# Performance work log

Hardware: AMD Instinct MI355X
Metric: run time of the kernel (lower is better)

The kernel has to match this reference:

```python
import jax, jax.numpy as jnp
import numpy as np

B, C, H, W = 32, 512, 32, 32
D = C // 8

def setup_inputs() -> dict:
    key = jax.random.key(0)
    ks = jax.random.split(key, 5)
    return {
        "x": jax.random.normal(ks[0], (B, C, H, W), dtype=jnp.float32),
        "w1": jax.random.normal(ks[1], (D, C), dtype=jnp.float32) * (1.0 / np.sqrt(C)),
        "b1": jax.random.normal(ks[2], (D,), dtype=jnp.float32) * 0.01,
        "w2": jax.random.normal(ks[3], (C, C), dtype=jnp.float32) * (1.0 / np.sqrt(C)),
        "b2": jax.random.normal(ks[4], (C,), dtype=jnp.float32) * 0.01,
    }

def reference(x, w1, b1, w2, b2):
    b, c, h, w = x.shape
    n = h * w
    xf = x.reshape(b, c, n)                                   # [B,C,N]
    # 1x1 convs == channel-mixing GEMMs; conv1 is shared for q and k
    qk = jnp.einsum('bcn,dc->bdn', xf, w1) + b1[None, :, None]  # [B,D,N]
    v = jnp.einsum('bcn,oc->bon', xf, w2) + b2[None, :, None]   # [B,C,N]
    q = qk.transpose(0, 2, 1)                                 # [B,N,D]
    attn = jax.nn.softmax(jnp.einsum('bnd,bdm->bnm', q, qk), axis=-1)  # [B,N,N]
    out = jnp.einsum('bnm,bcm->bnc', attn, v)                 # [B,N,C]
    # Faithful quirk: original views [B,N,C] directly as [B,C,H,W] (no transpose)
    return x + out.reshape(b, c, h, w)
```

## Files before the change

### kernel.cpp

```cpp
#include <hip/hip_runtime.h>
#include <hip/hip_bf16.h>
#include <math.h>

#define B_ 32
#define C_ 512
#define N_ 1024
#define D_ 64
#define OPAD 640

typedef __attribute__((ext_vector_type(4))) float f32x4;
typedef __attribute__((ext_vector_type(4))) float float4v;
typedef __attribute__((ext_vector_type(8))) __bf16 bf16x8;

#define MFMA16(a, b, c) __builtin_amdgcn_mfma_f32_16x16x32_bf16((a), (b), (c), 0, 0, 0)

__device__ inline void load_lds16(const void* g, void* l) {
    __builtin_amdgcn_global_load_lds(
        (const __attribute__((address_space(1))) void*)g,
        (__attribute__((address_space(3))) void*)l, 16, 0, 0);
}

__global__ void k_cast_weights(const float* __restrict__ w1,
                               const float* __restrict__ w2,
                               __hip_bfloat16* __restrict__ Wbf) {
    int idx = blockIdx.x * 256 + threadIdx.x;
    if (idx >= OPAD * C_) return;
    int m = idx >> 9;
    int k = idx & (C_ - 1);
    float val = (m < D_) ? w1[m * C_ + k]
              : (m < D_ + C_) ? w2[(m - D_) * C_ + k] : 0.0f;
    Wbf[idx] = __float2bfloat16(val);
}

__global__ __launch_bounds__(256) void k_transpose_cast(
        const float* __restrict__ x, __hip_bfloat16* __restrict__ xT) {
    __shared__ float tile[64][68];
    int b = blockIdx.z;
    int n0 = blockIdx.x * 64;
    int c0 = blockIdx.y * 64;
    int t = threadIdx.x;
    const float* xb = x + (size_t)b * (C_ * N_);
#pragma unroll
    for (int i = 0; i < 4; i++) {
        int c = i * 16 + (t >> 4);
        int nc = (t & 15) * 4;
        *(float4v*)&tile[c][nc] =
            *(const float4v*)(xb + (size_t)(c0 + c) * N_ + n0 + nc);
    }
    __syncthreads();
    __hip_bfloat16* xTb = xT + (size_t)b * (N_ * C_);
#pragma unroll
    for (int i = 0; i < 2; i++) {
        int n = i * 32 + (t >> 3);
        int cs = (t & 7) * 8;
        alignas(16) __hip_bfloat16 tmp[8];
#pragma unroll
        for (int j = 0; j < 8; j++)
            tmp[j] = __float2bfloat16(tile[cs + j][n]);
        *(bf16x8*)(xTb + (size_t)(n0 + n) * C_ + c0 + cs) = *(bf16x8*)tmp;
    }
}

__global__ __launch_bounds__(256) void k_gemm_qkv(
        const __hip_bfloat16* __restrict__ Wbf,
        const __hip_bfloat16* __restrict__ xT,
        const float* __restrict__ b1, const float* __restrict__ b2,
        __hip_bfloat16* __restrict__ qkT, __hip_bfloat16* __restrict__ v) {
    __shared__ __hip_bfloat16 As[128 * 64];
    __shared__ __hip_bfloat16 Bs[128 * 64];
    __shared__ __hip_bfloat16 epi[4][16][72];
    int b = blockIdx.x;
    int t = threadIdx.x;
    int wave = t >> 6, lane = t & 63, lr = lane & 15, quad = lane >> 4;
    int wm = wave >> 1, wn = wave & 1;
    int m_blk = blockIdx.z * 128;
    int n_blk = blockIdx.y * 128;
    const __hip_bfloat16* xTb = xT + (size_t)b * (N_ * C_);

    f32x4 acc[4][4] = {};
    for (int kk = 0; kk < C_; kk += 64) {
#pragma unroll
        for (int i = 0; i < 4; i++) {
            int id = i * 256 + t;
            int r = id >> 3, cx = id & 7;
            int gc = cx ^ (r & 7);
            load_lds16(Wbf + (size_t)(m_blk + r) * C_ + kk + gc * 8, &As[id * 8]);
            load_lds16(xTb + (size_t)(n_blk + r) * C_ + kk + gc * 8, &Bs[id * 8]);
        }
        __syncthreads();
#pragma unroll
        for (int h = 0; h < 2; h++) {
            bf16x8 af[4], bfr[4];
#pragma unroll
            for (int i = 0; i < 4; i++) {
                int ra = wm * 64 + i * 16 + lr;
                int rb = wn * 64 + i * 16 + lr;
                int q = h * 4 + quad;
                af[i]  = *(const bf16x8*)&As[ra * 64 + (q ^ (lr & 7)) * 8];
                bfr[i] = *(const bf16x8*)&Bs[rb * 64 + (q ^ (lr & 7)) * 8];
            }
#pragma unroll
            for (int mt = 0; mt < 4; mt++)
#pragma unroll
                for (int nt = 0; nt < 4; nt++)
                    acc[mt][nt] = MFMA16(af[mt], bfr[nt], acc[mt][nt]);
        }
        __syncthreads();
    }

#pragma unroll
    for (int mt = 0; mt < 4; mt++) {
        int m_frag = m_blk + wm * 64 + mt * 16;
        if (m_frag >= D_ + C_) continue;
        int m0 = m_frag + quad * 4;
        if (m_frag < D_) {
#pragma unroll
            for (int nt = 0; nt < 4; nt++) {
                int n = n_blk + wn * 64 + nt * 16 + lr;
                alignas(8) __hip_bfloat16 tmp[4];
#pragma unroll
                for (int r = 0; r < 4; r++)
                    tmp[r] = __float2bfloat16(acc[mt][nt][r] + b1[m0 + r]);
                *reinterpret_cast<short4*>(qkT + ((size_t)b * N_ + n) * D_ + m0) =
                    *reinterpret_cast<short4*>(tmp);
            }
        } else {
#pragma unroll
            for (int nt = 0; nt < 4; nt++) {
#pragma unroll
                for (int r = 0; r < 4; r++) {
                    int c = m0 - D_ + r;
                    epi[wave][quad * 4 + r][nt * 16 + lr] =
                        __float2bfloat16(acc[mt][nt][r] + b2[c]);
                }
            }
            int cbase = m_frag - D_;
            int row = lane >> 2;
#pragma unroll
            for (int it = 0; it < 2; it++) {
                int col = it * 32 + (lane & 3) * 8;
                bf16x8 frag = *(const bf16x8*)&epi[wave][row][col];
                *(bf16x8*)(v + (size_t)(b * C_ + cbase + row) * N_
                             + n_blk + wn * 64 + col) = frag;
            }
        }
    }
}

__global__ __launch_bounds__(512, 2) void k_fused_attn(
        const __hip_bfloat16* __restrict__ qkT,
        const __hip_bfloat16* __restrict__ v,
        const float* __restrict__ x, float* __restrict__ out) {
    __shared__ char smem[155648];
    __hip_bfloat16* Ks  = (__hip_bfloat16*)smem;
    __hip_bfloat16* Vs0 = (__hip_bfloat16*)(smem + 8192);
    __hip_bfloat16* Vs1 = (__hip_bfloat16*)(smem + 73728);
    __hip_bfloat16* Ps  = (__hip_bfloat16*)(smem + 139264);
    float* Obuf = (float*)smem;
    float* Rs   = (float*)(smem + 66560);

    int b = blockIdx.x;
    int t = threadIdx.x;
    int wave = t >> 6, lane = t & 63, lr = lane & 15, quad = lane >> 4;
    int wm = wave >> 2, wn = wave & 3;
    int n_blk = blockIdx.y * 128;
    const __hip_bfloat16* qb = qkT + (size_t)b * (N_ * D_);
    const __hip_bfloat16* vb = v + (size_t)b * (C_ * N_);

    {
        int r = t >> 3, cxx = t & 7, gc = cxx ^ (r & 7);
        load_lds16(qb + (size_t)r * D_ + gc * 8, &Ks[t * 8]);
    }
#pragma unroll
    for (int i = 0; i < 8; i++) {
        int id = i * 512 + t;
        int r = id >> 3, cxx = id & 7, gc = cxx ^ (r & 7);
        load_lds16(vb + (size_t)r * N_ + gc * 8, &Vs0[id * 8]);
    }

    union bfu { bf16x8 v; __hip_bfloat16 h[8]; };
    bf16x8 bq[2];
    float shift;
    {
        int nq = n_blk + wave * 16 + lr;
        bq[0] = *(const bf16x8*)(qb + (size_t)nq * D_ + quad * 8);
        bq[1] = *(const bf16x8*)(qb + (size_t)nq * D_ + 32 + quad * 8);
        float sq = 0.f;
#pragma unroll
        for (int dh = 0; dh < 2; dh++) {
            bfu u; u.v = bq[dh];
#pragma unroll
            for (int j = 0; j < 8; j++) {
                float qv = __bfloat162float(u.h[j]);
                sq += qv * qv;
            }
        }
        sq += __shfl_xor(sq, 16);
        sq += __shfl_xor(sq, 32);
        shift = sq;
    }

    f32x4 acc[4][8] = {};
    float rsum = 0.f;

    __syncthreads();

    for (int tt = 0; tt < 16; ++tt) {
        int kk = tt * 64;
        __hip_bfloat16* Vcur = (tt & 1) ? Vs1 : Vs0;
        __hip_bfloat16* Vnxt = (tt & 1) ? Vs0 : Vs1;

        if (tt < 15) {
#pragma unroll
            for (int i = 0; i < 8; i++) {
                int id = i * 512 + t;
                int r = id >> 3, cxx = id & 7, gc = cxx ^ (r & 7);
                load_lds16(vb + (size_t)r * N_ + kk + 64 + gc * 8, &Vnxt[id * 8]);
            }
        }

#pragma unroll
        for (int mi = 0; mi < 4; mi++) {
            int m = mi * 16 + lr;
            bf16x8 ak0 = *(const bf16x8*)&Ks[m * 64 + ((quad) ^ (lr & 7)) * 8];
            bf16x8 ak1 = *(const bf16x8*)&Ks[m * 64 + ((4 + quad) ^ (lr & 7)) * 8];
            f32x4 s = {};
            s = MFMA16(ak0, bq[0], s);
            s = MFMA16(ak1, bq[1], s);
            alignas(8) __hip_bfloat16 tmp[4];
#pragma unroll
            for (int r = 0; r < 4; r++) {
                float e = __expf(s[r] - shift);
                rsum += e;
                tmp[r] = __float2bfloat16(e);
            }
            int n = wave * 16 + lr;
            int cx2 = mi * 2 + (quad >> 1);
            int slot = cx2 ^ (lr & 7);
            *(short4*)&Ps[n * 64 + slot * 8 + (quad & 1) * 4] = *(short4*)tmp;
        }

        asm volatile("s_waitcnt lgkmcnt(0)" ::: "memory");
        __builtin_amdgcn_s_barrier();
        __builtin_amdgcn_sched_barrier(0);

        if (tt < 15) {
            int r = t >> 3, cxx = t & 7, gc = cxx ^ (r & 7);
            load_lds16(qb + (size_t)(kk + 64 + r) * D_ + gc * 8, &Ks[t * 8]);
        }

#pragma unroll
        for (int h = 0; h < 2; h++) {
            bf16x8 af[4];
#pragma unroll
            for (int i = 0; i < 4; i++) {
                int ra = wm * 64 + i * 16 + lr;
                af[i] = *(const bf16x8*)&Ps[ra * 64 + ((h * 4 + quad) ^ (lr & 7)) * 8];
            }
#pragma unroll
            for (int g = 0; g < 2; g++) {
                bf16x8 bfr[4];
#pragma unroll
                for (int j = 0; j < 4; j++) {
                    int rb = wn * 128 + (g * 4 + j) * 16 + lr;
                    bfr[j] = *(const bf16x8*)&Vcur[rb * 64 + ((h * 4 + quad) ^ (lr & 7)) * 8];
                }
#pragma unroll
                for (int mt = 0; mt < 4; mt++)
#pragma unroll
                    for (int j = 0; j < 4; j++)
                        acc[mt][g * 4 + j] = MFMA16(af[mt], bfr[j], acc[mt][g * 4 + j]);
            }
        }
        __syncthreads();
    }

    rsum += __shfl_xor(rsum, 16);
    rsum += __shfl_xor(rsum, 32);
    if (quad == 0) Rs[wave * 16 + lr] = 1.0f / rsum;

    const float* xb = x + (size_t)b * (N_ * C_);
    float* ob = out + (size_t)b * (N_ * C_);
#pragma unroll
    for (int h = 0; h < 2; h++) {
#pragma unroll
        for (int g = 0; g < 2; g++) {
            __syncthreads();
            if (wm == h && (wn >> 1) == g) {
#pragma unroll
                for (int mt = 0; mt < 4; mt++)
#pragma unroll
                    for (int nt = 0; nt < 8; nt++)
#pragma unroll
                        for (int r = 0; r < 4; r++)
                            Obuf[(mt * 16 + quad * 4 + r) * 260
                                 + (wn & 1) * 128 + nt * 16 + lr] =
                                acc[mt][nt][r];
            }
            __syncthreads();
#pragma unroll
            for (int i = 0; i < 8; i++) {
                int id = i * 512 + t;
                int rl = id >> 6;
                int c4 = (id & 63) * 4;
                int n = n_blk + h * 64 + rl;
                float ri = Rs[h * 64 + rl];
                float4v o = *(const float4v*)&Obuf[rl * 260 + c4];
                size_t gidx = (size_t)n * C_ + g * 256 + c4;
                float4v xv = *(const float4v*)(xb + gidx);
                float4v res;
                res.x = xv.x + ri * o.x;
                res.y = xv.y + ri * o.y;
                res.z = xv.z + ri * o.z;
                res.w = xv.w + ri * o.w;
                *(float4v*)(ob + gidx) = res;
            }
        }
    }
}

extern "C" void kernel_launch(void* const* d_in, const int* in_sizes, int n_in,
                              void* d_out, int out_size, void* d_ws, size_t ws_size,
                              hipStream_t stream) {
    const float* x  = (const float*)d_in[0];
    const float* w1 = (const float*)d_in[1];
    const float* b1 = (const float*)d_in[2];
    const float* w2 = (const float*)d_in[3];
    const float* b2 = (const float*)d_in[4];
    float* out = (float*)d_out;

    char* ws = (char*)d_ws;
    size_t off = 0;
    __hip_bfloat16* Wbf = (__hip_bfloat16*)(ws + off); off += (size_t)OPAD * C_ * 2;
    __hip_bfloat16* xT  = (__hip_bfloat16*)(ws + off); off += (size_t)B_ * N_ * C_ * 2;
    __hip_bfloat16* qkT = (__hip_bfloat16*)(ws + off); off += (size_t)B_ * N_ * D_ * 2;
    __hip_bfloat16* v   = (__hip_bfloat16*)(ws + off); off += (size_t)B_ * C_ * N_ * 2;

    hipLaunchKernelGGL(k_cast_weights, dim3((OPAD * C_ + 255) / 256), dim3(256), 0, stream,
                       w1, w2, Wbf);
    hipLaunchKernelGGL(k_transpose_cast, dim3(N_ / 64, C_ / 64, B_), dim3(256), 0, stream,
                       x, xT);
    hipLaunchKernelGGL(k_gemm_qkv, dim3(B_, N_ / 128, OPAD / 128), dim3(256), 0, stream,
                       Wbf, xT, b1, b2, qkT, v);
    hipLaunchKernelGGL(k_fused_attn, dim3(B_, N_ / 128), dim3(512), 0, stream,
                       qkT, v, x, out);
}
```

Before: 207.7 us.

## Fuse weight cast into transpose, double-buffer QKV GEMM, stream V from global

```diff
diff --git a/kernel.cpp b/kernel.cpp
--- a/kernel.cpp
+++ b/kernel.cpp
@@ -20,25 +20,37 @@
         (__attribute__((address_space(3))) void*)l, 16, 0, 0);
 }
 
-__global__ void k_cast_weights(const float* __restrict__ w1,
-                               const float* __restrict__ w2,
-                               __hip_bfloat16* __restrict__ Wbf) {
-    int idx = blockIdx.x * 256 + threadIdx.x;
-    if (idx >= OPAD * C_) return;
-    int m = idx >> 9;
-    int k = idx & (C_ - 1);
-    float val = (m < D_) ? w1[m * C_ + k]
-              : (m < D_ + C_) ? w2[(m - D_) * C_ + k] : 0.0f;
-    Wbf[idx] = __float2bfloat16(val);
-}
-
 __global__ __launch_bounds__(256) void k_transpose_cast(
-        const float* __restrict__ x, __hip_bfloat16* __restrict__ xT) {
+        const float* __restrict__ x,
+        const float* __restrict__ w1, const float* __restrict__ w2,
+        __hip_bfloat16* __restrict__ xT, __hip_bfloat16* __restrict__ Wbf) {
     __shared__ float tile[64][68];
     int b = blockIdx.z;
     int n0 = blockIdx.x * 64;
     int c0 = blockIdx.y * 64;
     int t = threadIdx.x;
+
+    int lid = blockIdx.x + 16 * blockIdx.y + 128 * blockIdx.z;
+    if (lid < 160) {
+        int base = lid * 2048 + t * 8;
+        int m = base >> 9, k = base & 511;
+        alignas(16) __hip_bfloat16 wtmp[8];
+        if (m < D_ + C_) {
+            const float* s = (m < D_) ? w1 + (size_t)m * C_ + k
+                                      : w2 + (size_t)(m - D_) * C_ + k;
+            float4v a = *(const float4v*)s;
+            float4v c = *(const float4v*)(s + 4);
+            wtmp[0] = __float2bfloat16(a.x); wtmp[1] = __float2bfloat16(a.y);
+            wtmp[2] = __float2bfloat16(a.z); wtmp[3] = __float2bfloat16(a.w);
+            wtmp[4] = __float2bfloat16(c.x); wtmp[5] = __float2bfloat16(c.y);
+            wtmp[6] = __float2bfloat16(c.z); wtmp[7] = __float2bfloat16(c.w);
+        } else {
+#pragma unroll
+            for (int j = 0; j < 8; j++) wtmp[j] = __float2bfloat16(0.0f);
+        }
+        *(bf16x8*)(Wbf + base) = *(bf16x8*)wtmp;
+    }
+
     const float* xb = x + (size_t)b * (C_ * N_);
 #pragma unroll
     for (int i = 0; i < 4; i++) {
@@ -66,9 +78,8 @@
         const __hip_bfloat16* __restrict__ xT,
         const float* __restrict__ b1, const float* __restrict__ b2,
         __hip_bfloat16* __restrict__ qkT, __hip_bfloat16* __restrict__ v) {
-    __shared__ __hip_bfloat16 As[128 * 64];
-    __shared__ __hip_bfloat16 Bs[128 * 64];
-    __shared__ __hip_bfloat16 epi[4][16][72];
+    __shared__ __hip_bfloat16 AB[2][2][128 * 64];
+    __hip_bfloat16* epi = &AB[0][0][0];
     int b = blockIdx.x;
     int t = threadIdx.x;
     int wave = t >> 6, lane = t & 63, lr = lane & 15, quad = lane >> 4;
@@ -77,17 +88,31 @@
     int n_blk = blockIdx.y * 128;
     const __hip_bfloat16* xTb = xT + (size_t)b * (N_ * C_);
 
+#pragma unroll
+    for (int i = 0; i < 4; i++) {
+        int id = i * 256 + t;
+        int r = id >> 3, cx = id & 7, gc = cx ^ (r & 7);
+        load_lds16(Wbf + (size_t)(m_blk + r) * C_ + gc * 8, &AB[0][0][id * 8]);
+        load_lds16(xTb + (size_t)(n_blk + r) * C_ + gc * 8, &AB[0][1][id * 8]);
+    }
+    __syncthreads();
+
     f32x4 acc[4][4] = {};
-    for (int kk = 0; kk < C_; kk += 64) {
-#pragma unroll
-        for (int i = 0; i < 4; i++) {
-            int id = i * 256 + t;
-            int r = id >> 3, cx = id & 7;
-            int gc = cx ^ (r & 7);
-            load_lds16(Wbf + (size_t)(m_blk + r) * C_ + kk + gc * 8, &As[id * 8]);
-            load_lds16(xTb + (size_t)(n_blk + r) * C_ + kk + gc * 8, &Bs[id * 8]);
-        }
-        __syncthreads();
+    for (int tt = 0; tt < 8; tt++) {
+        const __hip_bfloat16* As = AB[tt & 1][0];
+        const __hip_bfloat16* Bs = AB[tt & 1][1];
+        if (tt < 7) {
+            int kk = (tt + 1) * 64;
+            __hip_bfloat16* An = AB[(tt + 1) & 1][0];
+            __hip_bfloat16* Bn = AB[(tt + 1) & 1][1];
+#pragma unroll
+            for (int i = 0; i < 4; i++) {
+                int id = i * 256 + t;
+                int r = id >> 3, cx = id & 7, gc = cx ^ (r & 7);
+                load_lds16(Wbf + (size_t)(m_blk + r) * C_ + kk + gc * 8, &An[id * 8]);
+                load_lds16(xTb + (size_t)(n_blk + r) * C_ + kk + gc * 8, &Bn[id * 8]);
+            }
+        }
 #pragma unroll
         for (int h = 0; h < 2; h++) {
             bf16x8 af[4], bfr[4];
@@ -130,7 +155,7 @@
 #pragma unroll
                 for (int r = 0; r < 4; r++) {
                     int c = m0 - D_ + r;
-                    epi[wave][quad * 4 + r][nt * 16 + lr] =
+                    epi[(wave * 16 + quad * 4 + r) * 72 + nt * 16 + lr] =
                         __float2bfloat16(acc[mt][nt][r] + b2[c]);
                 }
             }
@@ -139,7 +164,7 @@
 #pragma unroll
             for (int it = 0; it < 2; it++) {
                 int col = it * 32 + (lane & 3) * 8;
-                bf16x8 frag = *(const bf16x8*)&epi[wave][row][col];
+                bf16x8 frag = *(const bf16x8*)&epi[(wave * 16 + row) * 72 + col];
                 *(bf16x8*)(v + (size_t)(b * C_ + cbase + row) * N_
                              + n_blk + wn * 64 + col) = frag;
             }
@@ -151,13 +176,13 @@
         const __hip_bfloat16* __restrict__ qkT,
         const __hip_bfloat16* __restrict__ v,
         const float* __restrict__ x, float* __restrict__ out) {
-    __shared__ char smem[155648];
-    __hip_bfloat16* Ks  = (__hip_bfloat16*)smem;
-    __hip_bfloat16* Vs0 = (__hip_bfloat16*)(smem + 8192);
-    __hip_bfloat16* Vs1 = (__hip_bfloat16*)(smem + 73728);
-    __hip_bfloat16* Ps  = (__hip_bfloat16*)(smem + 139264);
+    __shared__ char smem[67072];
+    __hip_bfloat16* Ks0 = (__hip_bfloat16*)smem;
+    __hip_bfloat16* Ks1 = (__hip_bfloat16*)(smem + 8192);
+    __hip_bfloat16* Ps0 = (__hip_bfloat16*)(smem + 16384);
+    __hip_bfloat16* Ps1 = (__hip_bfloat16*)(smem + 49152);
     float* Obuf = (float*)smem;
-    float* Rs   = (float*)(smem + 66560);
+    __shared__ float Rs[128];
 
     int b = blockIdx.x;
     int t = threadIdx.x;
@@ -169,13 +194,7 @@
 
     {
         int r = t >> 3, cxx = t & 7, gc = cxx ^ (r & 7);
-        load_lds16(qb + (size_t)r * D_ + gc * 8, &Ks[t * 8]);
-    }
-#pragma unroll
-    for (int i = 0; i < 8; i++) {
-        int id = i * 512 + t;
-        int r = id >> 3, cxx = id & 7, gc = cxx ^ (r & 7);
-        load_lds16(vb + (size_t)r * N_ + gc * 8, &Vs0[id * 8]);
+        load_lds16(qb + (size_t)r * D_ + gc * 8, &Ks0[t * 8]);
     }
 
     union bfu { bf16x8 v; __hip_bfloat16 h[8]; };
@@ -206,24 +225,21 @@
     __syncthreads();
 
     for (int tt = 0; tt < 16; ++tt) {
-        int kk = tt * 64;
-        __hip_bfloat16* Vcur = (tt & 1) ? Vs1 : Vs0;
-        __hip_bfloat16* Vnxt = (tt & 1) ? Vs0 : Vs1;
+        const int kk = tt * 64;
+        __hip_bfloat16* Kst = (tt & 1) ? Ks1 : Ks0;
+        __hip_bfloat16* Ksn = (tt & 1) ? Ks0 : Ks1;
+        __hip_bfloat16* Pst = (tt & 1) ? Ps1 : Ps0;
 
         if (tt < 15) {
-#pragma unroll
-            for (int i = 0; i < 8; i++) {
-                int id = i * 512 + t;
-                int r = id >> 3, cxx = id & 7, gc = cxx ^ (r & 7);
-                load_lds16(vb + (size_t)r * N_ + kk + 64 + gc * 8, &Vnxt[id * 8]);
-            }
+            int r = t >> 3, cxx = t & 7, gc = cxx ^ (r & 7);
+            load_lds16(qb + (size_t)(kk + 64 + r) * D_ + gc * 8, &Ksn[t * 8]);
         }
 
 #pragma unroll
         for (int mi = 0; mi < 4; mi++) {
             int m = mi * 16 + lr;
-            bf16x8 ak0 = *(const bf16x8*)&Ks[m * 64 + ((quad) ^ (lr & 7)) * 8];
-            bf16x8 ak1 = *(const bf16x8*)&Ks[m * 64 + ((4 + quad) ^ (lr & 7)) * 8];
+            bf16x8 ak0 = *(const bf16x8*)&Kst[m * 64 + ((quad) ^ (lr & 7)) * 8];
+            bf16x8 ak1 = *(const bf16x8*)&Kst[m * 64 + ((4 + quad) ^ (lr & 7)) * 8];
             f32x4 s = {};
             s = MFMA16(ak0, bq[0], s);
             s = MFMA16(ak1, bq[1], s);
@@ -237,17 +253,10 @@
             int n = wave * 16 + lr;
             int cx2 = mi * 2 + (quad >> 1);
             int slot = cx2 ^ (lr & 7);
-            *(short4*)&Ps[n * 64 + slot * 8 + (quad & 1) * 4] = *(short4*)tmp;
-        }
-
-        asm volatile("s_waitcnt lgkmcnt(0)" ::: "memory");
-        __builtin_amdgcn_s_barrier();
-        __builtin_amdgcn_sched_barrier(0);
-
-        if (tt < 15) {
-            int r = t >> 3, cxx = t & 7, gc = cxx ^ (r & 7);
-            load_lds16(qb + (size_t)(kk + 64 + r) * D_ + gc * 8, &Ks[t * 8]);
-        }
+            *(short4*)&Pst[n * 64 + slot * 8 + (quad & 1) * 4] = *(short4*)tmp;
+        }
+
+        __syncthreads();
 
 #pragma unroll
         for (int h = 0; h < 2; h++) {
@@ -255,7 +264,7 @@
 #pragma unroll
             for (int i = 0; i < 4; i++) {
                 int ra = wm * 64 + i * 16 + lr;
-                af[i] = *(const bf16x8*)&Ps[ra * 64 + ((h * 4 + quad) ^ (lr & 7)) * 8];
+                af[i] = *(const bf16x8*)&Pst[ra * 64 + ((h * 4 + quad) ^ (lr & 7)) * 8];
             }
 #pragma unroll
             for (int g = 0; g < 2; g++) {
@@ -263,7 +272,8 @@
 #pragma unroll
                 for (int j = 0; j < 4; j++) {
                     int rb = wn * 128 + (g * 4 + j) * 16 + lr;
-                    bfr[j] = *(const bf16x8*)&Vcur[rb * 64 + ((h * 4 + quad) ^ (lr & 7)) * 8];
+                    bfr[j] = *(const bf16x8*)(vb + (size_t)rb * N_ + kk
+                                              + (h * 4 + quad) * 8);
                 }
 #pragma unroll
                 for (int mt = 0; mt < 4; mt++)
@@ -272,7 +282,6 @@
                         acc[mt][g * 4 + j] = MFMA16(af[mt], bfr[j], acc[mt][g * 4 + j]);
             }
         }
-        __syncthreads();
     }
 
     rsum += __shfl_xor(rsum, 16);
@@ -336,10 +345,8 @@
     __hip_bfloat16* qkT = (__hip_bfloat16*)(ws + off); off += (size_t)B_ * N_ * D_ * 2;
     __hip_bfloat16* v   = (__hip_bfloat16*)(ws + off); off += (size_t)B_ * C_ * N_ * 2;
 
-    hipLaunchKernelGGL(k_cast_weights, dim3((OPAD * C_ + 255) / 256), dim3(256), 0, stream,
-                       w1, w2, Wbf);
     hipLaunchKernelGGL(k_transpose_cast, dim3(N_ / 64, C_ / 64, B_), dim3(256), 0, stream,
-                       x, xT);
+                       x, w1, w2, xT, Wbf);
     hipLaunchKernelGGL(k_gemm_qkv, dim3(B_, N_ / 128, OPAD / 128), dim3(256), 0, stream,
                        Wbf, xT, b1, b2, qkT, v);
     hipLaunchKernelGGL(k_fused_attn, dim3(B_, N_ / 128), dim3(512), 0, stream,
```

Result: slower. 241.3 us (+16.2%).
